# Optimization experiments

Measured on AMD Instinct MI355X. Metric: run time of the kernel, lower is better.

The kernel has to match this reference:

```python
import jax, jax.numpy as jnp
import numpy as np

PI = 3.141592653589793


def setup_inputs() -> dict:
    key = jax.random.key(0)
    k1, k2, k3, k4 = jax.random.split(key, 4)
    B, D, Q, L, C = 8192, 4096, 16, 24, 512
    features = jax.random.normal(k1, (B, D), dtype=jnp.float32)
    projection_w = jax.random.normal(k2, (Q, D), dtype=jnp.float32) * (1.0 / np.sqrt(D))
    projection_b = jnp.zeros((Q,), dtype=jnp.float32)
    vqc_weights = jax.random.uniform(k3, (L, Q, 3), dtype=jnp.float32, minval=0.0, maxval=2.0 * PI)
    linear_w = jax.random.normal(k4, (Q, C), dtype=jnp.float32) * 0.1
    linear_b = jnp.zeros((C,), dtype=jnp.float32)
    return {
        "features": features,
        "projection_w": projection_w,
        "projection_b": projection_b,
        "vqc_weights": vqc_weights,
        "linear_w": linear_w,
        "linear_b": linear_b,
    }


def _vqc_forward(angles, vqc_weights):
    # angles: (B, Q) data-encoding RY angles; vqc_weights: (L, Q, 3)
    # Per-qubit Bloch-vector simulation (no entanglement).
    # Start |0> -> Bloch (0,0,1); RY(a) gives (sin a, 0, cos a).
    x = jnp.sin(angles)
    y = jnp.zeros_like(angles)
    z = jnp.cos(angles)

    def layer(carry, w):
        x, y, z = carry
        phi, theta, omega = w[:, 0], w[:, 1], w[:, 2]  # each (Q,), broadcast over B
        # RZ(phi): rotate about Z
        cp, sp = jnp.cos(phi), jnp.sin(phi)
        x1 = x * cp - y * sp
        y1 = x * sp + y * cp
        # RY(theta): rotate about Y
        ct, st = jnp.cos(theta), jnp.sin(theta)
        x2 = x1 * ct + z * st
        z2 = -x1 * st + z * ct
        # RZ(omega)
        co, so = jnp.cos(omega), jnp.sin(omega)
        x3 = x2 * co - y1 * so
        y3 = x2 * so + y1 * co
        return (x3, y3, z2), None

    (x, y, z), _ = jax.lax.scan(layer, (x, y, z), vqc_weights)
    return z  # <Z> expectation per qubit, (B, Q)


def reference(features, projection_w, projection_b, vqc_weights, linear_w, linear_b):
    # classical projection to per-qubit angles, squashed to (-pi, pi)
    proj = features @ projection_w.T + projection_b  # (B, Q)
    angles = PI * jnp.tanh(proj)
    qubits = _vqc_forward(angles, vqc_weights)  # (B, Q)
    return qubits @ linear_w + linear_b  # (B, C)
```

## Files before the change

### kernel.cpp

```cpp
#include <hip/hip_runtime.h>
#include <hip/hip_bf16.h>

constexpr int D  = 4096;
constexpr int Q  = 16;
constexpr int L  = 24;
constexpr int C  = 512;
constexpr int RB = 32;
constexpr int KC = 256;
constexpr int NCH = D / KC;
constexpr int FSTRIDE = KC + 4;
constexpr float PI_F = 3.14159265358979323846f;

constexpr int OFF_FEAT0 = 0;
constexpr int SZ_FEAT   = RB * FSTRIDE;
constexpr int OFF_FEAT1 = OFF_FEAT0 + SZ_FEAT;
constexpr int OFF_PW0   = OFF_FEAT1 + SZ_FEAT;
constexpr int SZ_PW     = Q * FSTRIDE;
constexpr int OFF_PW1   = OFF_PW0 + SZ_PW;
constexpr int OFF_TRIG  = OFF_PW1 + SZ_PW;
constexpr int SZ_TRIG   = L * Q * 6;
constexpr int OFF_QUB   = OFF_TRIG + SZ_TRIG;
constexpr int SZ_QUB    = RB * Q;
constexpr int LDS_FLOATS = OFF_QUB + SZ_QUB;
constexpr int OFF_RED   = OFF_FEAT0;

typedef const __attribute__((address_space(1))) void* gas_ptr;
typedef __attribute__((address_space(3))) void* las_ptr;

__device__ inline void glds16(const float* g, float* l) {
    __builtin_amdgcn_global_load_lds((gas_ptr)g, (las_ptr)l, 16, 0, 0);
}

__device__ inline void stage_chunk(const float* __restrict__ feat,
                                   const float* __restrict__ pw,
                                   float* lds, int row0, int c, int buf,
                                   int wave, int lane, int B) {
    float* fdst = lds + (buf ? OFF_FEAT1 : OFF_FEAT0);
    float* wdst = lds + (buf ? OFF_PW1 : OFF_PW0);
    const int kbase = c * KC;
    #pragma unroll
    for (int p = 0; p < 4; ++p) {
        const int r = p * 8 + wave;
        int rr = row0 + r; if (rr > B - 1) rr = B - 1;
        glds16(feat + (size_t)rr * D + kbase + lane * 4,
               fdst + r * FSTRIDE);
    }
    #pragma unroll
    for (int p = 0; p < 2; ++p) {
        const int q = p * 8 + wave;
        glds16(pw + (size_t)q * D + kbase + lane * 4,
               wdst + q * FSTRIDE);
    }
}

__global__ __launch_bounds__(512)
void vqc_fused(const float* __restrict__ feat,
               const float* __restrict__ pw,
               const float* __restrict__ pb,
               const float* __restrict__ vw,
               const float* __restrict__ lw,
               const float* __restrict__ lb,
               float* __restrict__ out, int B)
{
    __shared__ float lds[LDS_FLOATS];

    const int t    = threadIdx.x;
    const int wave = t >> 6;
    const int lane = t & 63;
    const int row0 = blockIdx.x * RB;

    const int qg = lane & 3;
    const int rg = (lane >> 2) & 7;
    const int kh = lane >> 5;

    stage_chunk(feat, pw, lds, row0, 0, 0, wave, lane, B);
    if (t < L * Q) {
        const float phi = vw[t * 3 + 0], th = vw[t * 3 + 1], om = vw[t * 3 + 2];
        float* tr = lds + OFF_TRIG + t * 6;
        tr[0] = cosf(phi); tr[1] = sinf(phi);
        tr[2] = cosf(th);  tr[3] = sinf(th);
        tr[4] = cosf(om);  tr[5] = sinf(om);
    }
    __syncthreads();

    float acc[4][4] = {};
    for (int c = 0; c < NCH; ++c) {
        const int buf = c & 1;
        if (c + 1 < NCH)
            stage_chunk(feat, pw, lds, row0, c + 1, buf ^ 1, wave, lane, B);

        const float* fb = lds + (buf ? OFF_FEAT1 : OFF_FEAT0);
        const float* wb = lds + (buf ? OFF_PW1 : OFF_PW0);
        const int k0w = wave * 32 + kh * 4;
        #pragma unroll
        for (int ii = 0; ii < 4; ++ii) {
            const int koff = k0w + ii * 8;
            float4 w4[4], f4[4];
            #pragma unroll
            for (int jq = 0; jq < 4; ++jq)
                w4[jq] = *(const float4*)(wb + (qg * 4 + jq) * FSTRIDE + koff);
            #pragma unroll
            for (int jr = 0; jr < 4; ++jr)
                f4[jr] = *(const float4*)(fb + (rg * 4 + jr) * FSTRIDE + koff);
            #pragma unroll
            for (int jq = 0; jq < 4; ++jq)
                #pragma unroll
                for (int jr = 0; jr < 4; ++jr) {
                    acc[jq][jr] = fmaf(w4[jq].x, f4[jr].x, acc[jq][jr]);
                    acc[jq][jr] = fmaf(w4[jq].y, f4[jr].y, acc[jq][jr]);
                    acc[jq][jr] = fmaf(w4[jq].z, f4[jr].z, acc[jq][jr]);
                    acc[jq][jr] = fmaf(w4[jq].w, f4[jr].w, acc[jq][jr]);
                }
        }
        __syncthreads();
    }

    {
        float* red = lds + OFF_RED;
        const int slot = wave * 2 + kh;
        #pragma unroll
        for (int jq = 0; jq < 4; ++jq)
            #pragma unroll
            for (int jr = 0; jr < 4; ++jr)
                red[slot * 512 + (rg * 4 + jr) * 16 + (qg * 4 + jq)] = acc[jq][jr];
    }
    __syncthreads();

    {
        const int r = t >> 4, q = t & 15;
        const float* red = lds + OFF_RED;
        float p = 0.f;
        #pragma unroll
        for (int i = 0; i < 16; ++i) p += red[i * 512 + r * 16 + q];
        p += pb[q];
        const float angle = PI_F * tanhf(p);
        float x = sinf(angle), y = 0.f, z = cosf(angle);
        const float* tr = lds + OFF_TRIG;
        #pragma unroll
        for (int l = 0; l < L; ++l) {
            const float* w6 = tr + (l * 16 + q) * 6;
            const float cp = w6[0], sp = w6[1];
            const float ct = w6[2], st = w6[3];
            const float co = w6[4], so = w6[5];
            const float x1 = x * cp - y * sp;
            const float y1 = x * sp + y * cp;
            const float x2 = x1 * ct + z * st;
            const float z2 = -x1 * st + z * ct;
            x = x2 * co - y1 * so;
            y = x2 * so + y1 * co;
            z = z2;
        }
        lds[OFF_QUB + r * 16 + q] = z;
    }
    __syncthreads();

    {
        const int cc = t;
        float wv[Q];
        #pragma unroll
        for (int q = 0; q < Q; ++q) wv[q] = lw[(size_t)q * C + cc];
        const float lbv = lb[cc];
        const float* qub = lds + OFF_QUB;
        #pragma unroll 4
        for (int r = 0; r < RB; ++r) {
            if (row0 + r >= B) break;
            float a2 = lbv;
            #pragma unroll
            for (int q = 0; q < Q; ++q) a2 = fmaf(qub[r * 16 + q], wv[q], a2);
            out[(size_t)(row0 + r) * C + cc] = a2;
        }
    }
}

extern "C" void kernel_launch(void* const* d_in, const int* in_sizes, int n_in,
                              void* d_out, int out_size, void* d_ws, size_t ws_size,
                              hipStream_t stream) {
    const float *feat = nullptr, *pw = nullptr, *pb = nullptr,
                *vw = nullptr, *lw = nullptr, *lb = nullptr;
    long long B = 0;
    bool ok = false;
    if (n_in == 6) {
        int imax = 0;
        for (int i = 1; i < 6; ++i)
            if ((long long)in_sizes[i] > (long long)in_sizes[imax]) imax = i;
        const long long scales[2] = {1, 4};
        for (int s = 0; s < 2 && !ok; ++s) {
            const long long sc = scales[s];
            int m[6] = {imax, -1, -1, -1, -1, -1};
            bool good = ((long long)in_sizes[imax] % (sc * D)) == 0;
            for (int i = 0; i < 6 && good; ++i) {
                if (i == imax) continue;
                long long e = (long long)in_sizes[i];
                if (e % sc) { good = false; break; }
                e /= sc;
                if      (e == 65536 && m[1] < 0) m[1] = i;
                else if (e == 16    && m[2] < 0) m[2] = i;
                else if (e == 1152  && m[3] < 0) m[3] = i;
                else if (e == 8192  && m[4] < 0) m[4] = i;
                else if (e == 512   && m[5] < 0) m[5] = i;
                else good = false;
            }
            if (good && m[1] >= 0 && m[2] >= 0 && m[3] >= 0 && m[4] >= 0 && m[5] >= 0) {
                feat = (const float*)d_in[m[0]];
                pw   = (const float*)d_in[m[1]];
                pb   = (const float*)d_in[m[2]];
                vw   = (const float*)d_in[m[3]];
                lw   = (const float*)d_in[m[4]];
                lb   = (const float*)d_in[m[5]];
                B = (long long)in_sizes[imax] / (sc * D);
                ok = true;
            }
        }
    }
    if (!ok) {
        feat = (const float*)d_in[0];
        pw   = (const float*)d_in[1];
        pb   = (const float*)d_in[2];
        vw   = (const float*)d_in[3];
        lw   = (const float*)d_in[4];
        lb   = (const float*)d_in[5];
        B = in_sizes[0] / D;
    }
    float* out = (float*)d_out;

    const int nblocks = (int)((B + RB - 1) / RB);
    dim3 grid(nblocks), block(512);
    hipLaunchKernelGGL(vqc_fused, grid, block, 0, stream,
                       feat, pw, pb, vw, lw, lb, out, (int)B);
}
```

Before: 211.6 us.

## Compute projection GEMM with split-bf16 MFMA, direct global loads, smaller row blocks

Replaces the LDS-staged FP32 FMA projection with MFMA 16x16x32 bf16 instructions. Each FP32 operand is split into a hi and a lo bf16 part, and three MFMAs per step (lo*hi, hi*lo, hi*hi) recover close to FP32 accuracy. Each wave handles one K slice and loads straight from global memory into registers, dropping the LDS double buffer. Row block size is halved to 16 so there are more blocks, and a launch-bounds occupancy hint is added. The cost is extra conversion ALU work and a small loss of precision from the missing lo*lo term.

```diff
diff --git a/kernel.cpp b/kernel.cpp
--- a/kernel.cpp
+++ b/kernel.cpp
@@ -1,59 +1,34 @@
 #include <hip/hip_runtime.h>
 #include <hip/hip_bf16.h>
+
+using short8  = __attribute__((ext_vector_type(8))) short;
+using floatx4 = __attribute__((ext_vector_type(4))) float;
 
 constexpr int D  = 4096;
 constexpr int Q  = 16;
 constexpr int L  = 24;
 constexpr int C  = 512;
-constexpr int RB = 32;
-constexpr int KC = 256;
-constexpr int NCH = D / KC;
-constexpr int FSTRIDE = KC + 4;
+constexpr int RB = 16;
+constexpr int NW = 8;
+constexpr int KW = D / NW;
+constexpr int NSTEP = KW / 32;
 constexpr float PI_F = 3.14159265358979323846f;
 
-constexpr int OFF_FEAT0 = 0;
-constexpr int SZ_FEAT   = RB * FSTRIDE;
-constexpr int OFF_FEAT1 = OFF_FEAT0 + SZ_FEAT;
-constexpr int OFF_PW0   = OFF_FEAT1 + SZ_FEAT;
-constexpr int SZ_PW     = Q * FSTRIDE;
-constexpr int OFF_PW1   = OFF_PW0 + SZ_PW;
-constexpr int OFF_TRIG  = OFF_PW1 + SZ_PW;
-constexpr int SZ_TRIG   = L * Q * 6;
-constexpr int OFF_QUB   = OFF_TRIG + SZ_TRIG;
-constexpr int SZ_QUB    = RB * Q;
-constexpr int LDS_FLOATS = OFF_QUB + SZ_QUB;
-constexpr int OFF_RED   = OFF_FEAT0;
-
-typedef const __attribute__((address_space(1))) void* gas_ptr;
-typedef __attribute__((address_space(3))) void* las_ptr;
-
-__device__ inline void glds16(const float* g, float* l) {
-    __builtin_amdgcn_global_load_lds((gas_ptr)g, (las_ptr)l, 16, 0, 0);
-}
-
-__device__ inline void stage_chunk(const float* __restrict__ feat,
-                                   const float* __restrict__ pw,
-                                   float* lds, int row0, int c, int buf,
-                                   int wave, int lane, int B) {
-    float* fdst = lds + (buf ? OFF_FEAT1 : OFF_FEAT0);
-    float* wdst = lds + (buf ? OFF_PW1 : OFF_PW0);
-    const int kbase = c * KC;
+__device__ inline void cvt8(const float4& v0, const float4& v1,
+                            short8& hi, short8& lo) {
+    const float f[8] = {v0.x, v0.y, v0.z, v0.w, v1.x, v1.y, v1.z, v1.w};
     #pragma unroll
-    for (int p = 0; p < 4; ++p) {
-        const int r = p * 8 + wave;
-        int rr = row0 + r; if (rr > B - 1) rr = B - 1;
-        glds16(feat + (size_t)rr * D + kbase + lane * 4,
-               fdst + r * FSTRIDE);
-    }
-    #pragma unroll
-    for (int p = 0; p < 2; ++p) {
-        const int q = p * 8 + wave;
-        glds16(pw + (size_t)q * D + kbase + lane * 4,
-               wdst + q * FSTRIDE);
+    for (int j = 0; j < 8; ++j) {
+        union { float f; unsigned u; } a, b, c;
+        a.f = f[j];
+        hi[j] = (short)(a.u >> 16);
+        b.u = a.u & 0xFFFF0000u;
+        c.f = a.f - b.f;
+        lo[j] = (short)(c.u >> 16);
     }
 }
 
-__global__ __launch_bounds__(512)
+__global__ __launch_bounds__(512, 4)
 void vqc_fused(const float* __restrict__ feat,
                const float* __restrict__ pw,
                const float* __restrict__ pb,
@@ -62,83 +37,59 @@
                const float* __restrict__ lb,
                float* __restrict__ out, int B)
 {
-    __shared__ float lds[LDS_FLOATS];
+    __shared__ float s_red[NW][RB][Q];
+    __shared__ float s_trig[L * Q * 6];
+    __shared__ float s_qub[RB][Q];
 
     const int t    = threadIdx.x;
     const int wave = t >> 6;
     const int lane = t & 63;
     const int row0 = blockIdx.x * RB;
+    const int mrow = lane & 15;
+    const int quad = lane >> 4;
 
-    const int qg = lane & 3;
-    const int rg = (lane >> 2) & 7;
-    const int kh = lane >> 5;
-
-    stage_chunk(feat, pw, lds, row0, 0, 0, wave, lane, B);
     if (t < L * Q) {
         const float phi = vw[t * 3 + 0], th = vw[t * 3 + 1], om = vw[t * 3 + 2];
-        float* tr = lds + OFF_TRIG + t * 6;
+        float* tr = s_trig + t * 6;
         tr[0] = cosf(phi); tr[1] = sinf(phi);
         tr[2] = cosf(th);  tr[3] = sinf(th);
         tr[4] = cosf(om);  tr[5] = sinf(om);
     }
+
+    int rr = row0 + mrow; if (rr >= B) rr = B - 1;
+    const float* ap = feat + (size_t)rr * D + wave * KW + quad * 8;
+    const float* bp = pw   + (size_t)mrow * D + wave * KW + quad * 8;
+
+    floatx4 acc = {0.f, 0.f, 0.f, 0.f};
+    #pragma unroll 4
+    for (int s = 0; s < NSTEP; ++s) {
+        const float4 a0 = *(const float4*)(ap + s * 32);
+        const float4 a1 = *(const float4*)(ap + s * 32 + 4);
+        const float4 b0 = *(const float4*)(bp + s * 32);
+        const float4 b1 = *(const float4*)(bp + s * 32 + 4);
+        short8 ah, al, bh, bl;
+        cvt8(a0, a1, ah, al);
+        cvt8(b0, b1, bh, bl);
+        acc = __builtin_amdgcn_mfma_f32_16x16x32_bf16(al, bh, acc, 0, 0, 0);
+        acc = __builtin_amdgcn_mfma_f32_16x16x32_bf16(ah, bl, acc, 0, 0, 0);
+        acc = __builtin_amdgcn_mfma_f32_16x16x32_bf16(ah, bh, acc, 0, 0, 0);
+    }
+    #pragma unroll
+    for (int i = 0; i < 4; ++i)
+        s_red[wave][quad * 4 + i][mrow] = acc[i];
     __syncthreads();
 
-    float acc[4][4] = {};
-    for (int c = 0; c < NCH; ++c) {
-        const int buf = c & 1;
-        if (c + 1 < NCH)
-            stage_chunk(feat, pw, lds, row0, c + 1, buf ^ 1, wave, lane, B);
-
-        const float* fb = lds + (buf ? OFF_FEAT1 : OFF_FEAT0);
-        const float* wb = lds + (buf ? OFF_PW1 : OFF_PW0);
-        const int k0w = wave * 32 + kh * 4;
-        #pragma unroll
-        for (int ii = 0; ii < 4; ++ii) {
-            const int koff = k0w + ii * 8;
-            float4 w4[4], f4[4];
-            #pragma unroll
-            for (int jq = 0; jq < 4; ++jq)
-                w4[jq] = *(const float4*)(wb + (qg * 4 + jq) * FSTRIDE + koff);
-            #pragma unroll
-            for (int jr = 0; jr < 4; ++jr)
-                f4[jr] = *(const float4*)(fb + (rg * 4 + jr) * FSTRIDE + koff);
-            #pragma unroll
-            for (int jq = 0; jq < 4; ++jq)
-                #pragma unroll
-                for (int jr = 0; jr < 4; ++jr) {
-                    acc[jq][jr] = fmaf(w4[jq].x, f4[jr].x, acc[jq][jr]);
-                    acc[jq][jr] = fmaf(w4[jq].y, f4[jr].y, acc[jq][jr]);
-                    acc[jq][jr] = fmaf(w4[jq].z, f4[jr].z, acc[jq][jr]);
-                    acc[jq][jr] = fmaf(w4[jq].w, f4[jr].w, acc[jq][jr]);
-                }
-        }
-        __syncthreads();
-    }
-
-    {
-        float* red = lds + OFF_RED;
-        const int slot = wave * 2 + kh;
-        #pragma unroll
-        for (int jq = 0; jq < 4; ++jq)
-            #pragma unroll
-            for (int jr = 0; jr < 4; ++jr)
-                red[slot * 512 + (rg * 4 + jr) * 16 + (qg * 4 + jq)] = acc[jq][jr];
-    }
-    __syncthreads();
-
-    {
+    if (t < RB * Q) {
         const int r = t >> 4, q = t & 15;
-        const float* red = lds + OFF_RED;
         float p = 0.f;
         #pragma unroll
-        for (int i = 0; i < 16; ++i) p += red[i * 512 + r * 16 + q];
+        for (int w = 0; w < NW; ++w) p += s_red[w][r][q];
         p += pb[q];
         const float angle = PI_F * tanhf(p);
         float x = sinf(angle), y = 0.f, z = cosf(angle);
-        const float* tr = lds + OFF_TRIG;
         #pragma unroll
         for (int l = 0; l < L; ++l) {
-            const float* w6 = tr + (l * 16 + q) * 6;
+            const float* w6 = s_trig + (l * 16 + q) * 6;
             const float cp = w6[0], sp = w6[1];
             const float ct = w6[2], st = w6[3];
             const float co = w6[4], so = w6[5];
@@ -150,24 +101,23 @@
             y = x2 * so + y1 * co;
             z = z2;
         }
-        lds[OFF_QUB + r * 16 + q] = z;
+        s_qub[r][q] = z;
     }
     __syncthreads();
 
     {
-        const int cc = t;
+        const int c = t;
         float wv[Q];
         #pragma unroll
-        for (int q = 0; q < Q; ++q) wv[q] = lw[(size_t)q * C + cc];
-        const float lbv = lb[cc];
-        const float* qub = lds + OFF_QUB;
+        for (int q = 0; q < Q; ++q) wv[q] = lw[(size_t)q * C + c];
+        const float lbv = lb[c];
         #pragma unroll 4
         for (int r = 0; r < RB; ++r) {
             if (row0 + r >= B) break;
             float a2 = lbv;
             #pragma unroll
-            for (int q = 0; q < Q; ++q) a2 = fmaf(qub[r * 16 + q], wv[q], a2);
-            out[(size_t)(row0 + r) * C + cc] = a2;
+            for (int q = 0; q < Q; ++q) a2 = fmaf(s_qub[r][q], wv[q], a2);
+            out[(size_t)(row0 + r) * C + c] = a2;
         }
     }
 }
```

New measurement: 206.5 us. -2.4%, faster.
